# Kernel optimization log

Measured on AMD Instinct MI355X. Metric: run time of the kernel, lower is better.

The kernel has to match this reference:

```python
import jax, jax.numpy as jnp
import numpy as np

BS, TS, NE, ED = 32, 64, 64, 96
E = 256        # attn_embed_dim
H = 4          # attn_n_heads
HD = E // H    # head dim
RNN_H = 256
N_ACT = 32
NA = 16        # n_agents


def setup_inputs():
    key = jax.random.key(0)
    ks = jax.random.split(key, 40)
    entities = jax.random.normal(ks[0], (BS, TS, NE, ED), jnp.float32)
    obs_mask = jax.random.randint(ks[1], (BS, TS, NE, NE), 0, 2).astype(jnp.float32)  # 1 = masked
    entity_mask = (jax.random.uniform(ks[2], (BS, TS, NE)) < 0.1).astype(jnp.float32)  # 1 = inactive
    hidden_state = jnp.zeros((BS * NA, RNN_H), jnp.float32)
    it = iter(range(3, 40))
    def lin(fi, fo):
        return jax.random.normal(ks[next(it)], (fi, fo), jnp.float32) / np.sqrt(fi).astype(np.float32)
    p = dict(
        fc1_w=lin(ED, E), fc1_b=jnp.zeros((E,), jnp.float32),
        attn_in_w=lin(E, 3 * E), attn_out_w=lin(E, E), attn_out_b=jnp.zeros((E,), jnp.float32),
        fc2_w=lin(2 * E, RNN_H), fc2_b=jnp.zeros((RNN_H,), jnp.float32),
        gru_w_ih=lin(RNN_H, 3 * RNN_H), gru_w_hh=lin(RNN_H, 3 * RNN_H),
        gru_b_ih=jnp.zeros((3 * RNN_H,), jnp.float32), gru_b_hh=jnp.zeros((3 * RNN_H,), jnp.float32),
        fc3_w=lin(RNN_H, N_ACT), fc3_b=jnp.zeros((N_ACT,), jnp.float32),
        fcmsg1_w=lin(ED, E), fcmsg1_b=jnp.zeros((E,), jnp.float32),
        lmsg_in_w=lin(E, 3 * E), lmsg_out_w=lin(E, E), lmsg_out_b=jnp.zeros((E,), jnp.float32),
        gmsg_in_w=lin(E, 3 * E), gmsg_out_w=lin(E, E), gmsg_out_b=jnp.zeros((E,), jnp.float32),
        gate_in_w=lin(E, 3 * E), gate_out_w=lin(E, E), gate_out_b=jnp.zeros((E,), jnp.float32),
        gatefc1_w=lin(ED, E), gatefc1_b=jnp.zeros((E,), jnp.float32),
        gatefc2_w=lin(E, 2), gatefc2_b=jnp.zeros((2,), jnp.float32),
    )
    return dict(entities=entities, obs_mask=obs_mask, entity_mask=entity_mask,
                hidden_state=hidden_state, **p)


def _attn(x, in_w, out_w, out_b, pre_mask, post_mask):
    """REFIL EntityAttentionLayer: n_queries = NA agent rows, masks use 1 = masked."""
    B, ne, e = x.shape
    q, k, v = jnp.split(x @ in_w, 3, axis=-1)                       # each [B, ne, E]
    q = q[:, :NA].reshape(B, NA, H, HD).transpose(0, 2, 1, 3)        # [B, H, NA, HD]
    k = k.reshape(B, ne, H, HD).transpose(0, 2, 1, 3)                # [B, H, ne, HD]
    v = v.reshape(B, ne, H, HD).transpose(0, 2, 1, 3)
    logits = jnp.einsum('bhqd,bhkd->bhqk', q, k) / jnp.asarray(np.sqrt(HD), x.dtype)
    m = pre_mask[:, None, :NA, :]                                    # [B, 1, NA, ne]
    logits = jnp.where(m > 0, jnp.asarray(-1e9, x.dtype), logits)
    # softmax; zeroing masked cols also reproduces torch's NaN->0 for fully-masked rows
    w = jax.nn.softmax(logits, axis=-1) * (1.0 - m)
    out = jnp.einsum('bhqk,bhkd->bhqd', w, v).transpose(0, 2, 1, 3).reshape(B, NA, e)
    out = out @ out_w + out_b
    return out * (1.0 - post_mask[..., None])                        # masked_fill(post_mask, 0)


def _forward(entities, obs_mask, entity_mask, hidden_state,
             fc1_w, fc1_b, attn_in_w, attn_out_w, attn_out_b, fc2_w, fc2_b,
             gru_w_ih, gru_w_hh, gru_b_ih, gru_b_hh, fc3_w, fc3_b,
             fcmsg1_w, fcmsg1_b, lmsg_in_w, lmsg_out_w, lmsg_out_b,
             gmsg_in_w, gmsg_out_w, gmsg_out_b, gate_in_w, gate_out_w, gate_out_b,
             gatefc1_w, gatefc1_b, gatefc2_w, gatefc2_b):
    bs, ts, ne, ed = entities.shape
    B = bs * ts
    ent = entities.reshape(B, ne, ed)
    om = obs_mask.reshape(B, ne, ne)
    em = entity_mask.reshape(B, ne)
    agent_mask = em[:, :NA]                                          # [B, NA]
    full_obs_mask = 1.0 - (1.0 - agent_mask[:, None, :]) * (1.0 - agent_mask[:, :, None])

    x1 = jax.nn.relu(ent @ fc1_w + fc1_b)
    x2 = _attn(x1, attn_in_w, attn_out_w, attn_out_b, om, agent_mask)          # [B, NA, E]

    x1_msg = jax.nn.relu(ent @ fcmsg1_w + fcmsg1_b)
    x1_gate = jax.nn.relu(ent @ gatefc1_w + gatefc1_b)
    x2_msg = _attn(x1_msg, lmsg_in_w, lmsg_out_w, lmsg_out_b, om, agent_mask)  # [B, NA, E]
    x2_gate = _attn(x1_gate, gate_in_w, gate_out_w, gate_out_b, om, agent_mask)
    x2_gate = x2_gate @ gatefc2_w + gatefc2_b                                   # [B, NA, 2]

    # argmax of softmax == argmax of logits; gate in {0,1}, non-differentiable
    gate = jnp.argmax(x2_gate, axis=-1).astype(entities.dtype)
    gated_msg = x2_msg * gate[..., None]
    global_msg = _attn(gated_msg, gmsg_in_w, gmsg_out_w, gmsg_out_b,
                       full_obs_mask, agent_mask)                               # [B, NA, E]

    x3 = jax.nn.relu(jnp.concatenate([x2, global_msg], axis=-1) @ fc2_w + fc2_b)
    x3 = x3.reshape(bs, ts, NA, RNN_H)

    # GRU recurrence over ts via scan; hidden flattened to [bs*NA, RNN_H]
    h0 = hidden_state.reshape(-1, RNN_H)
    xs = x3.transpose(1, 0, 2, 3).reshape(ts, bs * NA, RNN_H)

    def step(h, x):
        gi = x @ gru_w_ih + gru_b_ih
        gh = h @ gru_w_hh + gru_b_hh
        ir, iz, inn = jnp.split(gi, 3, axis=-1)
        hr, hz, hn = jnp.split(gh, 3, axis=-1)
        r = jax.nn.sigmoid(ir + hr)
        z = jax.nn.sigmoid(iz + hz)
        n = jnp.tanh(inn + r * hn)
        h_new = (1.0 - z) * n + z * h
        return h_new, h_new

    _, hs = jax.lax.scan(step, h0, xs)                               # [ts, bs*NA, RNN_H]
    hs = hs.reshape(ts, bs, NA, RNN_H).transpose(1, 0, 2, 3)         # [bs, ts, NA, RNN_H]

    q = hs @ fc3_w + fc3_b                                           # [bs, ts, NA, N_ACT]
    am = agent_mask.reshape(bs, ts, NA, 1)
    q = q * (1.0 - am)                                               # masked_fill(agent_mask, 0)
    return q, hs, x2_gate


def reference(entities, obs_mask, entity_mask, hidden_state,
              fc1_w, fc1_b, attn_in_w, attn_out_w, attn_out_b, fc2_w, fc2_b,
              gru_w_ih, gru_w_hh, gru_b_ih, gru_b_hh, fc3_w, fc3_b,
              fcmsg1_w, fcmsg1_b, lmsg_in_w, lmsg_out_w, lmsg_out_b,
              gmsg_in_w, gmsg_out_w, gmsg_out_b, gate_in_w, gate_out_w, gate_out_b,
              gatefc1_w, gatefc1_b, gatefc2_w, gatefc2_b):
    return _forward(entities, obs_mask, entity_mask, hidden_state,
                    fc1_w, fc1_b, attn_in_w, attn_out_w, attn_out_b, fc2_w, fc2_b,
                    gru_w_ih, gru_w_hh, gru_b_ih, gru_b_hh, fc3_w, fc3_b,
                    fcmsg1_w, fcmsg1_b, lmsg_in_w, lmsg_out_w, lmsg_out_b,
                    gmsg_in_w, gmsg_out_w, gmsg_out_b, gate_in_w, gate_out_w, gate_out_b,
                    gatefc1_w, gatefc1_b, gatefc2_w, gatefc2_b)
```

## Files before the change

kernel.cpp:

```cpp
#include <hip/hip_runtime.h>


#define DEV __device__ __forceinline__

typedef _Float16 f16x8 __attribute__((ext_vector_type(8)));
typedef _Float16 f16x4 __attribute__((ext_vector_type(4)));
typedef float    f32x4 __attribute__((ext_vector_type(4)));
typedef float    f32x16 __attribute__((ext_vector_type(16)));

DEV f32x4 mfma16(f16x8 a, f16x8 b, f32x4 c){
  return __builtin_amdgcn_mfma_f32_16x16x32_f16(a, b, c, 0, 0, 0);
}
DEV f32x16 mfma32(f16x8 a, f16x8 b, f32x16 c){
  return __builtin_amdgcn_mfma_f32_32x32x16_f16(a, b, c, 0, 0, 0);
}

template<int MODE> struct AB {
  f16x8 hi, lo;
  DEV void mf(const AB& b, f32x4& c) const {
    if constexpr (MODE){
      c = mfma16(lo, b.hi, c);
      c = mfma16(hi, b.lo, c);
    }
    c = mfma16(hi, b.hi, c);
  }
};

template<int MODE> DEV AB<MODE> ldW(const _Float16* p, int losz){
  AB<MODE> r; r.hi = *(const f16x8*)p;
  if constexpr (MODE) r.lo = *(const f16x8*)(p + losz);
  return r;
}
template<int MODE> DEV AB<MODE> ldL(const _Float16* ph, const _Float16* pl){
  AB<MODE> r; r.hi = *(const f16x8*)ph;
  if constexpr (MODE) r.lo = *(const f16x8*)pl;
  return r;
}
template<int MODE> DEV AB<MODE> ldF(const float* p){
  AB<MODE> r;
  f32x4 v0 = *(const f32x4*)p, v1 = *(const f32x4*)(p + 4);
#pragma unroll
  for (int i = 0; i < 4; ++i){
    float a = v0[i], b = v1[i];
    _Float16 ah = (_Float16)a, bh = (_Float16)b;
    r.hi[i] = ah; r.hi[i+4] = bh;
    if constexpr (MODE){
      r.lo[i]   = (_Float16)(a - (float)ah);
      r.lo[i+4] = (_Float16)(b - (float)bh);
    }
  }
  return r;
}
template<int MODE> DEV void stL(_Float16* ph, _Float16* pl, int idx, float v){
  _Float16 h = (_Float16)v;
  ph[idx] = h;
  if constexpr (MODE) pl[idx] = (_Float16)(v - (float)h);
}

struct WJobs {
  const float* src[15];
  unsigned off[15];
  int K[15], N[15], mode[15];
};

__global__ __launch_bounds__(256) void k0_conv(WJobs jb, char* ws){
  const int job = blockIdx.y;
  const int K = jb.K[job], N = jb.N[job];
  const int total = K * N;
  _Float16* dh = (_Float16*)(ws + jb.off[job]);
  const float* src = jb.src[job];
  const int m = jb.mode[job];
  for (int idx = blockIdx.x*256 + threadIdx.x; idx < total; idx += gridDim.x*256){
    int n = idx / K, k = idx - n*K;
    float v = src[(size_t)k*N + n];
    _Float16 h = (_Float16)v;
    dh[idx] = h;
    if (m) dh[total + idx] = (_Float16)(v - (float)h);
  }
}

__global__ __launch_bounds__(256) void k0w_gate(
    const float* __restrict__ Wout, const float* __restrict__ Wg2,
    const float* __restrict__ bo,   const float* __restrict__ Win,
    _Float16* __restrict__ wveff, float* __restrict__ beff)
{
  __shared__ float weff_s[256*2];
  const int tid = threadIdx.x;
  {
    float a0 = 0.f, a1 = 0.f;
    const float* wr = Wout + (size_t)tid*256;
    for (int f = 0; f < 256; ++f){ float x = wr[f]; a0 += x*Wg2[2*f]; a1 += x*Wg2[2*f+1]; }
    weff_s[tid*2] = a0; weff_s[tid*2+1] = a1;
  }
  if (tid < 2){
    float s = 0.f;
    for (int f = 0; f < 256; ++f) s += bo[f]*Wg2[2*f + tid];
    beff[tid] = s;
  }
  __syncthreads();
  {
    const int j = tid;
    for (int n = 0; n < 16; ++n){
      float v = 0.f;
      if (n < 8){
        int h = n >> 1, c = n & 1;
        const float* wr = Win + (size_t)j*768 + 512 + h*64;
        const float* we = weff_s + (h*64)*2 + c;
        for (int d = 0; d < 64; ++d) v += wr[d]*we[2*d];
      }
      _Float16 hi = (_Float16)v;
      wveff[n*256 + j] = hi;
      wveff[16*256 + n*256 + j] = (_Float16)(v - (float)hi);
    }
  }
}

__global__ __launch_bounds__(512) void k1_all(
    const float* __restrict__ ent, const float* __restrict__ om, const float* __restrict__ em,
    const _Float16* __restrict__ W1a, const float* __restrict__ b1a,
    const _Float16* __restrict__ WINa,
    const _Float16* __restrict__ WOUTa, const float* __restrict__ boa,
    float* __restrict__ x2outa,
    const _Float16* __restrict__ W1b, const float* __restrict__ b1b,
    const _Float16* __restrict__ WINb,
    const _Float16* __restrict__ WOUTb, const float* __restrict__ bob,
    float* __restrict__ x2outb,
    const _Float16* __restrict__ W1g, const float* __restrict__ b1g,
    const _Float16* __restrict__ WINg,
    const _Float16* __restrict__ WVEFF,
    const float* __restrict__ beff, const float* __restrict__ gb2,
    float* __restrict__ og, float* __restrict__ gate)
{
  const int tid = threadIdx.x;
  const int w = tid >> 6, lg = (tid >> 4) & 3, li = tid & 15;
  extern __shared__ char smem[];

  if (blockIdx.x < 2048){
    const int br = blockIdx.x >> 10;
    const int p  = blockIdx.x & 1023;
    const int bb2[2] = { 2*p, 2*p + 1 };
    const _Float16* W1   = br ? W1b   : W1a;
    const float*    b1   = br ? b1b   : b1a;
    const _Float16* WIN  = br ? WINb  : WINa;
    const _Float16* WOUT = br ? WOUTb : WOUTa;
    const float*    bo   = br ? bob   : boa;
    float*          x2out= br ? x2outb: x2outa;

    const int wi = w & 3, ih = w >> 2;
    const int l = tid & 63;
    const int r32 = l & 31, kh = (l >> 5)*8;

    _Float16* x1   = (_Float16*)smem;
    _Float16* Ks   = (_Float16*)(smem + 67584);
    _Float16* Vs   = (_Float16*)(smem + 86016);
    _Float16* Qful = (_Float16*)(smem + 104448);
    float*    lgs  = (float*)(smem + 121344);
    _Float16* Ps   = (_Float16*)(smem + 130560);
    _Float16* outp = (_Float16*)(smem + 135168);

    {
      const int b = bb2[ih];
      _Float16* x1p = x1 + ih*16896;
      const int mt = wi & 1, ntb = (wi >> 1)*4;
      f32x16 acc0 = 0.f, acc1 = 0.f, acc2 = 0.f, acc3 = 0.f;
#pragma unroll
      for (int kk = 0; kk < 6; ++kk){
        AB<0> a = ldF<0>(ent + ((size_t)b*64 + mt*32 + r32)*96 + kk*16 + kh);
        f16x8 B0 = *(const f16x8*)(W1 + (size_t)((ntb + 0)*32 + r32)*96 + kk*16 + kh);
        f16x8 B1 = *(const f16x8*)(W1 + (size_t)((ntb + 1)*32 + r32)*96 + kk*16 + kh);
        f16x8 B2 = *(const f16x8*)(W1 + (size_t)((ntb + 2)*32 + r32)*96 + kk*16 + kh);
        f16x8 B3 = *(const f16x8*)(W1 + (size_t)((ntb + 3)*32 + r32)*96 + kk*16 + kh);
        acc0 = mfma32(a.hi, B0, acc0);
        acc1 = mfma32(a.hi, B1, acc1);
        acc2 = mfma32(a.hi, B2, acc2);
        acc3 = mfma32(a.hi, B3, acc3);
      }
#pragma unroll
      for (int s = 0; s < 4; ++s){
        const f32x16& ac = (s == 0) ? acc0 : (s == 1) ? acc1 : (s == 2) ? acc2 : acc3;
        int col = (ntb + s)*32 + r32;
        float bias = b1[col];
#pragma unroll
        for (int reg = 0; reg < 16; ++reg){
          int row = (reg & 3) + 8*(reg >> 2) + 4*(l >> 5);
          x1p[(mt*32 + row)*264 + col] = (_Float16)fmaxf(ac[reg] + bias, 0.f);
        }
      }
    }
    __syncthreads();

    {
      f32x16 acc = 0.f;
      const int itq = r32 >> 4, qr = r32 & 15;
      for (int kk = 0; kk < 16; ++kk){
        f16x8 A = *(const f16x8*)(x1 + itq*16896 + qr*264 + kk*16 + kh);
        f16x8 B = *(const f16x8*)(WIN + (size_t)(w*32 + r32)*256 + kk*16 + kh);
        acc = mfma32(A, B, acc);
      }
#pragma unroll
      for (int reg = 0; reg < 16; ++reg){
        int row = (reg & 3) + 8*(reg >> 2) + 4*(l >> 5);
        Qful[(row >> 4)*4224 + (row & 15)*264 + w*32 + r32] = (_Float16)acc[reg];
      }
    }
    __syncthreads();

    for (int h = 0; h < 4; ++h){
      if (w < 4){
        const int kt = w >> 1, dt = w & 1;
        f32x16 acc0 = 0.f, acc1 = 0.f;
        for (int kk = 0; kk < 16; ++kk){
          int ao = (kt*32 + r32)*264 + kk*16 + kh;
          f16x8 A0 = *(const f16x8*)(x1 + ao);
          f16x8 A1 = *(const f16x8*)(x1 + 16896 + ao);
          f16x8 B = *(const f16x8*)(WIN + (size_t)(256 + 64*h + dt*32 + r32)*256 + kk*16 + kh);
          acc0 = mfma32(A0, B, acc0);
          acc1 = mfma32(A1, B, acc1);
        }
#pragma unroll
        for (int reg = 0; reg < 16; ++reg){
          int row = (reg & 3) + 8*(reg >> 2) + 4*(l >> 5);
          Ks[(kt*32 + row)*72 + dt*32 + r32]        = (_Float16)acc0[reg];
          Ks[4608 + (kt*32 + row)*72 + dt*32 + r32] = (_Float16)acc1[reg];
        }
      } else {
        const int wv = w - 4;
        const int kt = wv >> 1, dt = wv & 1;
        f32x16 acc0 = 0.f, acc1 = 0.f;
        for (int kk = 0; kk < 16; ++kk){
          int ao = (kt*32 + r32)*264 + kk*16 + kh;
          f16x8 A0 = *(const f16x8*)(x1 + ao);
          f16x8 A1 = *(const f16x8*)(x1 + 16896 + ao);
          f16x8 B = *(const f16x8*)(WIN + (size_t)(512 + 64*h + dt*32 + r32)*256 + kk*16 + kh);
          acc0 = mfma32(A0, B, acc0);
          acc1 = mfma32(A1, B, acc1);
        }
#pragma unroll
        for (int rr = 0; rr < 4; ++rr){
          f16x4 p0, p1;
#pragma unroll
          for (int q4 = 0; q4 < 4; ++q4){
            p0[q4] = (_Float16)acc0[rr*4 + q4];
            p1[q4] = (_Float16)acc1[rr*4 + q4];
          }
          int key = kt*32 + rr*8 + 4*(l >> 5);
          *(f16x4*)(Vs + (dt*32 + r32)*72 + key)        = p0;
          *(f16x4*)(Vs + 4608 + (dt*32 + r32)*72 + key) = p1;
        }
      }
      __syncthreads();
      {
        const int b = bb2[ih];
        f32x4 acc = 0.f;
#pragma unroll
        for (int kk = 0; kk < 2; ++kk){
          f16x8 A = *(const f16x8*)(Qful + ih*4224 + li*264 + 64*h + kk*32 + lg*8);
          f16x8 B = *(const f16x8*)(Ks + ih*4608 + (16*wi + li)*72 + kk*32 + lg*8);
          acc = mfma16(A, B, acc);
        }
#pragma unroll
        for (int j = 0; j < 4; ++j){
          int q = 4*lg + j, key = 16*wi + li;
          float v = acc[j] * 0.125f;
          float m = om[((size_t)b*64 + q)*64 + key];
          if (m > 0.f) v = -1e9f;
          lgs[ih*1152 + q*72 + key] = v;
        }
      }
      __syncthreads();
      {
        const int it = tid >> 8, q = (tid >> 4) & 15, i16 = tid & 15;
        const int b = bb2[it];
        float pv[4], mx = -3e38f;
#pragma unroll
        for (int u = 0; u < 4; ++u){ pv[u] = lgs[it*1152 + q*72 + i16 + 16*u]; mx = fmaxf(mx, pv[u]); }
#pragma unroll
        for (int d = 1; d < 16; d <<= 1) mx = fmaxf(mx, __shfl_xor(mx, d, 16));
        float s = 0.f;
#pragma unroll
        for (int u = 0; u < 4; ++u){ pv[u] = expf(pv[u] - mx); s += pv[u]; }
#pragma unroll
        for (int d = 1; d < 16; d <<= 1) s += __shfl_xor(s, d, 16);
#pragma unroll
        for (int u = 0; u < 4; ++u){
          int key = i16 + 16*u;
          float m = om[((size_t)b*64 + q)*64 + key];
          Ps[it*1152 + q*72 + key] = (_Float16)((pv[u]/s)*(1.f - m));
        }
      }
      __syncthreads();
      {
        f32x4 acc = 0.f;
#pragma unroll
        for (int kk = 0; kk < 2; ++kk){
          f16x8 A = *(const f16x8*)(Ps + ih*1152 + li*72 + kk*32 + lg*8);
          f16x8 B = *(const f16x8*)(Vs + ih*4608 + (16*wi + li)*72 + kk*32 + lg*8);
          acc = mfma16(A, B, acc);
        }
#pragma unroll
        for (int j = 0; j < 4; ++j)
          outp[ih*4224 + (4*lg + j)*264 + 64*h + 16*wi + li] = (_Float16)acc[j];
      }
      __syncthreads();
    }

    {
      f32x16 acc = 0.f;
      const int ito = r32 >> 4, qr = r32 & 15;
      for (int kk = 0; kk < 16; ++kk){
        f16x8 A = *(const f16x8*)(outp + ito*4224 + qr*264 + kk*16 + kh);
        f16x8 B = *(const f16x8*)(WOUT + (size_t)(w*32 + r32)*256 + kk*16 + kh);
        acc = mfma32(A, B, acc);
      }
      int col = w*32 + r32;
      float bias = bo[col];
#pragma unroll
      for (int reg = 0; reg < 16; ++reg){
        int row = (reg & 3) + 8*(reg >> 2) + 4*(l >> 5);
        int it2 = row >> 4, q2 = row & 15;
        const int b = bb2[it2];
        float v = (acc[reg] + bias) * (1.f - em[(size_t)b*64 + q2]);
        x2out[((size_t)b*16 + q2)*256 + col] = v;
      }
    }
    return;
  }

  {
    constexpr int W1SZ = 96*256, WINSZ = 256*768, WVSZ = 16*256;
    const int b = blockIdx.x - 2048;
    const int l = tid & 63;
    const int r32 = l & 31, kh = (l >> 5)*8;

    char* sp = smem;
    _Float16* x1h = (_Float16*)sp; sp += 64*264*2;
    _Float16* x1l = (_Float16*)sp; sp += 64*264*2;
    _Float16* Kh  = (_Float16*)sp; sp += 64*72*2;
    _Float16* Kl  = (_Float16*)sp; sp += 64*72*2;
    _Float16* Qh  = (_Float16*)sp; sp += 16*264*2;
    _Float16* Ql  = (_Float16*)sp; sp += 16*264*2;
    float*    lgs = (float*)sp;    sp += 16*72*4;
    float*    Ps  = (float*)sp;    sp += 16*66*4;
    float*    v2s = (float*)sp;    sp += 64*18*4;
    float*  ogacc = (float*)sp;    sp += 32*4;
    float*  Kpart = (float*)sp;    sp += 8192*4;

    {
      const int mt = w & 1, ntb = (w >> 1)*2;
      f32x16 acc0 = 0.f, acc1 = 0.f;
#pragma unroll
      for (int kk = 0; kk < 6; ++kk){
        AB<1> a = ldF<1>(ent + ((size_t)b*64 + mt*32 + r32)*96 + kk*16 + kh);
#pragma unroll
        for (int s = 0; s < 2; ++s){
          const _Float16* bp = W1g + (size_t)((ntb + s)*32 + r32)*96 + kk*16 + kh;
          f16x8 Bh = *(const f16x8*)bp;
          f16x8 Bl = *(const f16x8*)(bp + W1SZ);
          f32x16& ac = s ? acc1 : acc0;
          ac = mfma32(a.lo, Bh, ac);
          ac = mfma32(a.hi, Bl, ac);
          ac = mfma32(a.hi, Bh, ac);
        }
      }
#pragma unroll
      for (int s = 0; s < 2; ++s){
        const f32x16& ac = s ? acc1 : acc0;
        int col = (ntb + s)*32 + r32;
        float bias = b1g[col];
#pragma unroll
        for (int reg = 0; reg < 16; ++reg){
          int row = (reg & 3) + 8*(reg >> 2) + 4*(l >> 5);
          stL<1>(x1h, x1l, (mt*32 + row)*264 + col, fmaxf(ac[reg] + bias, 0.f));
        }
      }
    }
    if (tid < 32) ogacc[tid] = 0.f;
    __syncthreads();

    {
#pragma unroll
      for (int s = 0; s < 2; ++s){
        int nt = w + s*8;
        f32x4 acc = 0.f;
        for (int kk = 0; kk < 8; ++kk){
          int ao = li*264 + kk*32 + lg*8;
          AB<1> a = ldL<1>(x1h + ao, x1l + ao);
          AB<1> bb = ldW<1>(WINg + (size_t)(nt*16 + li)*256 + kk*32 + lg*8, WINSZ);
          a.mf(bb, acc);
        }
#pragma unroll
        for (int j = 0; j < 4; ++j)
          stL<1>(Qh, Ql, (4*lg + j)*264 + nt*16 + li, acc[j]);
      }
      if (w < 4){
        f32x4 acc = 0.f;
        for (int kk = 0; kk < 8; ++kk){
          int ao = (w*16 + li)*264 + kk*32 + lg*8;
          AB<1> a = ldL<1>(x1h + ao, x1l + ao);
          AB<1> bb = ldW<1>(WVEFF + (size_t)li*256 + kk*32 + lg*8, WVSZ);
          a.mf(bb, acc);
        }
#pragma unroll
        for (int j = 0; j < 4; ++j)
          v2s[(w*16 + 4*lg + j)*18 + li] = acc[j];
      }
    }
    __syncthreads();

    for (int h = 0; h < 4; ++h){
      {
        const int t = w & 3, kt = t >> 1, dt = t & 1, khalf = w >> 2;
        f32x16 acc = 0.f;
#pragma unroll
        for (int k8 = 0; k8 < 8; ++k8){
          int ko = (khalf*8 + k8)*16 + kh;
          int ao = (kt*32 + r32)*264 + ko;
          f16x8 ah = *(const f16x8*)(x1h + ao);
          f16x8 al = *(const f16x8*)(x1l + ao);
          const _Float16* bp = WINg + (size_t)(256 + h*64 + dt*32 + r32)*256 + ko;
          f16x8 Bh = *(const f16x8*)bp;
          f16x8 Bl = *(const f16x8*)(bp + WINSZ);
          acc = mfma32(al, Bh, acc);
          acc = mfma32(ah, Bl, acc);
          acc = mfma32(ah, Bh, acc);
        }
#pragma unroll
        for (int reg = 0; reg < 16; ++reg){
          int row = (reg & 3) + 8*(reg >> 2) + 4*(l >> 5);
          Kpart[((khalf*4 + t)*32 + row)*32 + r32] = acc[reg];
        }
      }
      __syncthreads();
      {
        for (int e = tid; e < 4096; e += 512){
          float s2 = Kpart[e] + Kpart[4096 + e];
          int t2 = e >> 10, idx = e & 1023, row = idx >> 5, col = idx & 31;
          stL<1>(Kh, Kl, ((t2 >> 1)*32 + row)*72 + (t2 & 1)*32 + col, s2);
        }
      }
      __syncthreads();
      if (w < 4){
        f32x4 acc = 0.f;
#pragma unroll
        for (int kk = 0; kk < 2; ++kk){
          int ao = li*264 + h*64 + kk*32 + lg*8;
          AB<1> a = ldL<1>(Qh + ao, Ql + ao);
          int bo_ = (16*w + li)*72 + kk*32 + lg*8;
          AB<1> bb = ldL<1>(Kh + bo_, Kl + bo_);
          a.mf(bb, acc);
        }
#pragma unroll
        for (int j = 0; j < 4; ++j){
          int q = 4*lg + j, key = 16*w + li;
          float v = acc[j] * 0.125f;
          float m = om[((size_t)b*64 + q)*64 + key];
          if (m > 0.f) v = -1e9f;
          lgs[q*72 + key] = v;
        }
      }
      __syncthreads();
      if (tid < 256){
        int q = tid >> 4, i16 = tid & 15;
        float pv[4], mx = -3e38f;
#pragma unroll
        for (int u = 0; u < 4; ++u){ pv[u] = lgs[q*72 + i16 + 16*u]; mx = fmaxf(mx, pv[u]); }
#pragma unroll
        for (int d = 1; d < 16; d <<= 1) mx = fmaxf(mx, __shfl_xor(mx, d, 16));
        float s = 0.f;
#pragma unroll
        for (int u = 0; u < 4; ++u){ pv[u] = expf(pv[u] - mx); s += pv[u]; }
#pragma unroll
        for (int d = 1; d < 16; d <<= 1) s += __shfl_xor(s, d, 16);
#pragma unroll
        for (int u = 0; u < 4; ++u){
          int key = i16 + 16*u;
          float m = om[((size_t)b*64 + q)*64 + key];
          Ps[q*66 + key] = (pv[u]/s)*(1.f - m);
        }
      }
      __syncthreads();
      if (tid < 256){
        int q = tid >> 4, l16 = tid & 15;
        float a0 = 0.f, a1 = 0.f;
#pragma unroll
        for (int u = 0; u < 4; ++u){
          int k = l16 + 16*u;
          float p2 = Ps[q*66 + k];
          a0 += p2 * v2s[k*18 + h*2];
          a1 += p2 * v2s[k*18 + h*2 + 1];
        }
#pragma unroll
        for (int d = 1; d < 16; d <<= 1){ a0 += __shfl_xor(a0, d, 16); a1 += __shfl_xor(a1, d, 16); }
        if (l16 == 0){ ogacc[q*2] += a0; ogacc[q*2 + 1] += a1; }
      }
      __syncthreads();
    }
    if (tid < 16){
      int q = tid;
      float am = em[(size_t)b*64 + q];
      float g0 = (1.f - am)*(ogacc[2*q]     + beff[0]) + gb2[0];
      float g1 = (1.f - am)*(ogacc[2*q + 1] + beff[1]) + gb2[1];
      og[((size_t)b*16 + q)*2]     = g0;
      og[((size_t)b*16 + q)*2 + 1] = g1;
      gate[(size_t)b*16 + q] = (g1 > g0) ? 1.f : 0.f;
    }
  }
}

__global__ __launch_bounds__(512) void k2_global(
    const float* __restrict__ em,
    const float* __restrict__ x2, const float* __restrict__ x2m,
    const float* __restrict__ gate,
    const _Float16* __restrict__ GMIN, const _Float16* __restrict__ GMOUT, const float* __restrict__ gob,
    const _Float16* __restrict__ FC2T, const float* __restrict__ fc2b,
    const _Float16* __restrict__ GIHT, const float* __restrict__ gib,
    float* __restrict__ gi)
{
  const int p = blockIdx.x;
  const int tid = threadIdx.x;
  const int w = tid >> 6, lg = (tid >> 4) & 3, li = tid & 15;
  const int l = tid & 63;
  const int r32 = l & 31, kh = (l >> 5)*8;

  extern __shared__ char smem[];
  float*    gate_s = (float*)smem;
  _Float16* gm_s   = (_Float16*)(smem + 128);
  float*    lg2    = (float*)(smem + 17024);
  _Float16* P2     = (_Float16*)(smem + 20096);
  _Float16* outp   = (_Float16*)(smem + 22656);
  _Float16* x3_s   = (_Float16*)(smem + 39552);
  _Float16* Vtall  = (_Float16*)(smem + 56448);
  _Float16* Qall   = (_Float16*)(smem + 97408);
  _Float16* Kall   = (_Float16*)(smem + 114304);
  _Float16* cat_s  = (_Float16*)(smem + 97408);

  if (tid < 32){
    int it = tid >> 4, q = tid & 15;
    gate_s[it*16 + q] = gate[(size_t)(2*p + it)*16 + q];
  }
  __syncthreads();
#pragma unroll
  for (int it = 0; it < 2; ++it){
    const int b = 2*p + it;
    for (int idx = tid; idx < 4096; idx += 512){
      int q = idx >> 8, d = idx & 255;
      gm_s[it*4224 + q*264 + d] = (_Float16)(x2m[((size_t)b*16 + q)*256 + d] * gate_s[it*16 + q]);
    }
  }
  for (int idx = tid; idx < 10240; idx += 512) ((unsigned*)Vtall)[idx] = 0u;
  for (int idx = tid; idx < 2*16*40; idx += 512) P2[idx] = (_Float16)0.f;
  __syncthreads();

  {
    const int itq = r32 >> 4, qr = r32 & 15;
#pragma unroll
    for (int s = 0; s < 3; ++s){
      int nt = 3*w + s;
      f32x16 acc = 0.f;
      for (int kk = 0; kk < 16; ++kk){
        f16x8 A = *(const f16x8*)(gm_s + itq*4224 + qr*264 + kk*16 + kh);
        f16x8 B = *(const f16x8*)(GMIN + (size_t)(nt*32 + r32)*256 + kk*16 + kh);
        acc = mfma32(A, B, acc);
      }
      int sec = nt >> 3;
      int hcol = (nt & 7)*32 + r32;
#pragma unroll
      for (int reg = 0; reg < 16; ++reg){
        int row = (reg & 3) + 8*(reg >> 2) + 4*(l >> 5);
        int it2 = row >> 4, q2 = row & 15;
        _Float16 v = (_Float16)acc[reg];
        if (sec == 0)      Qall[it2*4224 + q2*264 + hcol] = v;
        else if (sec == 1) Kall[it2*4224 + q2*264 + hcol] = v;
        else               Vtall[it2*10240 + hcol*40 + q2] = v;
      }
    }
  }
  __syncthreads();

  for (int h = 0; h < 4; ++h){
    if (w < 2){
      const int it = w, b = 2*p + it;
      f32x4 acc = 0.f;
#pragma unroll
      for (int kk = 0; kk < 2; ++kk){
        f16x8 A = *(const f16x8*)(Qall + it*4224 + li*264 + 64*h + kk*32 + lg*8);
        f16x8 B = *(const f16x8*)(Kall + it*4224 + li*264 + 64*h + kk*32 + lg*8);
        acc = mfma16(A, B, acc);
      }
      float amk = em[(size_t)b*64 + li];
#pragma unroll
      for (int j = 0; j < 4; ++j){
        int q = 4*lg + j;
        float amq = em[(size_t)b*64 + q];
        float m = 1.f - (1.f - amq)*(1.f - amk);
        float v = acc[j]*0.125f;
        if (m > 0.f) v = -1e9f;
        lg2[it*384 + q*24 + li] = v;
      }
    }
    __syncthreads();
    if (tid < 256){
      int q = tid >> 4, key = tid & 15;
#pragma unroll
      for (int it = 0; it < 2; ++it){
        const int b = 2*p + it;
        float v = lg2[it*384 + q*24 + key];
        float mx = v;
#pragma unroll
        for (int d = 1; d < 16; d <<= 1) mx = fmaxf(mx, __shfl_xor(mx, d, 16));
        float pe = expf(v - mx);
        float s = pe;
#pragma unroll
        for (int d = 1; d < 16; d <<= 1) s += __shfl_xor(s, d, 16);
        float amq = em[(size_t)b*64 + q], amk = em[(size_t)b*64 + key];
        float m = 1.f - (1.f - amq)*(1.f - amk);
        P2[it*640 + q*40 + key] = (_Float16)((pe/s)*(1.f - m));
      }
    }
    __syncthreads();
    {
      const int it = w & 1, dt = w >> 1;
      f32x4 acc = 0.f;
      f16x8 A = *(const f16x8*)(P2 + it*640 + li*40 + lg*8);
      f16x8 B = *(const f16x8*)(Vtall + it*10240 + (size_t)(64*h + 16*dt + li)*40 + lg*8);
      acc = mfma16(A, B, acc);
#pragma unroll
      for (int j = 0; j < 4; ++j)
        outp[it*4224 + (4*lg + j)*264 + 64*h + 16*dt + li] = (_Float16)acc[j];
    }
    __syncthreads();
  }
  {
    const int ito = r32 >> 4, qr = r32 & 15;
    {
      int nt = w;
      f32x16 acc = 0.f;
      for (int kk = 0; kk < 16; ++kk){
        f16x8 A = *(const f16x8*)(outp + ito*4224 + qr*264 + kk*16 + kh);
        f16x8 B = *(const f16x8*)(GMOUT + (size_t)(nt*32 + r32)*256 + kk*16 + kh);
        acc = mfma32(A, B, acc);
      }
      int col = nt*32 + r32;
      float bias = gob[col];
#pragma unroll
      for (int reg = 0; reg < 16; ++reg){
        int row = (reg & 3) + 8*(reg >> 2) + 4*(l >> 5);
        int it2 = row >> 4, q2 = row & 15;
        float m = 1.f - em[(size_t)(2*p + it2)*64 + q2];
        cat_s[it2*8320 + q2*520 + 256 + col] = (_Float16)((acc[reg] + bias)*m);
      }
    }
#pragma unroll
    for (int it = 0; it < 2; ++it){
      const int b = 2*p + it;
      for (int idx = tid; idx < 4096; idx += 512){
        int q = idx >> 8, d = idx & 255;
        cat_s[it*8320 + q*520 + d] = (_Float16)(x2[((size_t)b*16 + q)*256 + d]);
      }
    }
  }
  __syncthreads();
  {
    const int ito = r32 >> 4, qr = r32 & 15;
    int nt = w;
    f32x16 acc = 0.f;
    for (int kk = 0; kk < 32; ++kk){
      f16x8 A = *(const f16x8*)(cat_s + ito*8320 + qr*520 + kk*16 + kh);
      f16x8 B = *(const f16x8*)(FC2T + (size_t)(nt*32 + r32)*512 + kk*16 + kh);
      acc = mfma32(A, B, acc);
    }
    int col = nt*32 + r32;
    float bias = fc2b[col];
#pragma unroll
    for (int reg = 0; reg < 16; ++reg){
      int row = (reg & 3) + 8*(reg >> 2) + 4*(l >> 5);
      int it2 = row >> 4, q2 = row & 15;
      x3_s[it2*4224 + q2*264 + col] = (_Float16)fmaxf(acc[reg] + bias, 0.f);
    }
  }
  __syncthreads();
  {
    const int r0 = ((2*p) >> 6)*16, t0 = (2*p) & 63;
    const int ito = r32 >> 4, qr = r32 & 15;
#pragma unroll
    for (int s = 0; s < 3; ++s){
      int nt = 3*w + s;
      f32x16 acc = 0.f;
      for (int kk = 0; kk < 16; ++kk){
        f16x8 A = *(const f16x8*)(x3_s + ito*4224 + qr*264 + kk*16 + kh);
        f16x8 B = *(const f16x8*)(GIHT + (size_t)(nt*32 + r32)*256 + kk*16 + kh);
        acc = mfma32(A, B, acc);
      }
      int col = nt*32 + r32;
      float bias = gib[col];
#pragma unroll
      for (int reg = 0; reg < 16; ++reg){
        int row = (reg & 3) + 8*(reg >> 2) + 4*(l >> 5);
        int it2 = row >> 4, q2 = row & 15;
        gi[((size_t)((r0 + q2)*64 + t0 + it2))*768 + col] = acc[reg] + bias;
      }
    }
  }
}

__global__ __launch_bounds__(512) void k3_gru(
    const _Float16* __restrict__ WHH, const float* __restrict__ bhh,
    const float* __restrict__ gi, const float* __restrict__ h0,
    float* __restrict__ hs)
{
  const int rb = blockIdx.x;
  const int row0 = rb * 16;
  const int tid = threadIdx.x;
  const int w = tid >> 6, lg = (tid >> 4) & 3, li = tid & 15;

  extern __shared__ char smem3[];
  _Float16* hf16 = (_Float16*)smem3;
  float* hf32 = (float*)(smem3 + 8448);
  float* gh   = (float*)(smem3 + 8448 + 16640);
  float* bhs  = (float*)(smem3 + 8448 + 16640 + 49664);

  for (int idx = tid; idx < 768; idx += 512) bhs[idx] = bhh[idx];
  for (int idx = tid; idx < 4096; idx += 512){
    int r = idx >> 8, d = idx & 255;
    float v = h0[(size_t)(row0 + r)*256 + d];
    hf32[r*260 + d] = v;
    hf16[r*264 + d] = (_Float16)v;
  }
  __syncthreads();

  const int er = tid >> 5;
  const int dd = (tid & 31) * 8;

  for (int t = 0; t < 64; ++t){
    const float* gp = gi + ((size_t)(row0 + er)*64 + t)*768 + dd;
    f32x4 gr[2], gz[2], gn[2];
#pragma unroll
    for (int v = 0; v < 2; ++v){
      gr[v] = *(const f32x4*)(gp + v*4);
      gz[v] = *(const f32x4*)(gp + 256 + v*4);
      gn[v] = *(const f32x4*)(gp + 512 + v*4);
    }
    f16x8 a[8];
#pragma unroll
    for (int kk = 0; kk < 8; ++kk)
      a[kk] = *(const f16x8*)(hf16 + li*264 + kk*32 + lg*8);
    f32x4 acc[6];
#pragma unroll
    for (int c = 0; c < 6; ++c) acc[c] = 0.f;
#pragma unroll
    for (int c = 0; c < 6; ++c){
      const _Float16* bp = WHH + (size_t)(w*96 + c*16 + li)*256 + lg*8;
#pragma unroll
      for (int kk = 0; kk < 8; ++kk)
        acc[c] = mfma16(a[kk], *(const f16x8*)(bp + kk*32), acc[c]);
    }
#pragma unroll
    for (int c = 0; c < 6; ++c){
      int col = w*96 + c*16 + li;
#pragma unroll
      for (int j = 0; j < 4; ++j)
        gh[(4*lg + j)*776 + col] = acc[c][j];
    }
    __syncthreads();
    {
      float* hp32 = hf32 + er*260 + dd;
      float* hsp  = hs + ((size_t)(rb*64 + t)*16 + er)*256 + dd;
      f16x8 hv8;
#pragma unroll
      for (int v = 0; v < 2; ++v){
        f32x4 xr = *(const f32x4*)(gh + er*776 +       dd + v*4);
        f32x4 xz = *(const f32x4*)(gh + er*776 + 256 + dd + v*4);
        f32x4 xn = *(const f32x4*)(gh + er*776 + 512 + dd + v*4);
        f32x4 hold = *(const f32x4*)(hp32 + v*4);
        f32x4 hout;
#pragma unroll
        for (int e = 0; e < 4; ++e){
          int d = dd + v*4 + e;
          float rr_ = 1.f/(1.f + __expf(-(gr[v][e] + xr[e] + bhs[d])));
          float zz  = 1.f/(1.f + __expf(-(gz[v][e] + xz[e] + bhs[256 + d])));
          float pre = gn[v][e] + rr_*(xn[e] + bhs[512 + d]);
          float nn  = 1.f - 2.f/(1.f + __expf(2.f*pre));
          float hv = (1.f - zz)*nn + zz*hold[e];
          hout[e] = hv;
          hv8[v*4 + e] = (_Float16)hv;
        }
        *(f32x4*)(hp32 + v*4) = hout;
        *(f32x4*)(hsp + v*4)  = hout;
      }
      *(f16x8*)(hf16 + er*264 + dd) = hv8;
    }
    __syncthreads();
  }
}

__global__ __launch_bounds__(256) void k4_q(
    const _Float16* __restrict__ FC3T, const float* __restrict__ fc3b,
    const float* __restrict__ em, const float* __restrict__ hs, float* __restrict__ qo)
{
  const int tid = threadIdx.x;
  const int w = tid >> 6, lg = (tid >> 4) & 3, li = tid & 15;
  const int rb = blockIdx.x*64 + 16*w;
  f32x4 acc[2];
#pragma unroll
  for (int c = 0; c < 2; ++c) acc[c] = 0.f;
  for (int kk = 0; kk < 8; ++kk){
    const float* ap = hs + (size_t)(rb + li)*256 + kk*32 + lg*8;
    f32x4 v0 = *(const f32x4*)ap, v1 = *(const f32x4*)(ap + 4);
    f16x8 A;
#pragma unroll
    for (int e = 0; e < 4; ++e){ A[e] = (_Float16)v0[e]; A[e+4] = (_Float16)v1[e]; }
#pragma unroll
    for (int c = 0; c < 2; ++c){
      f16x8 B = *(const f16x8*)(FC3T + (size_t)(16*c + li)*256 + kk*32 + lg*8);
      acc[c] = mfma16(A, B, acc[c]);
    }
  }
#pragma unroll
  for (int c = 0; c < 2; ++c){
    int col = 16*c + li;
    float bias = fc3b[col];
#pragma unroll
    for (int j = 0; j < 4; ++j){
      int row = rb + 4*lg + j;
      float am = em[(size_t)(row >> 4)*64 + (row & 15)];
      qo[(size_t)row*32 + col] = (acc[c][j] + bias)*(1.f - am);
    }
  }
}

extern "C" void kernel_launch(void* const* d_in, const int* in_sizes, int n_in,
                              void* d_out, int out_size, void* d_ws, size_t ws_size,
                              hipStream_t stream)
{
  constexpr size_t OFF_FC1T   = 0;
  constexpr size_t OFF_MSG1T  = 49152;
  constexpr size_t OFF_AINT   = 98304;
  constexpr size_t OFF_LINT   = 491520;
  constexpr size_t OFF_AOUTT  = 884736;
  constexpr size_t OFF_LOUTT  = 1015808;
  constexpr size_t OFF_GMINT  = 1146880;
  constexpr size_t OFF_GMOUTT = 1540096;
  constexpr size_t OFF_FC2T   = 1671168;
  constexpr size_t OFF_GIHT   = 1933312;
  constexpr size_t OFF_GHHT   = 2326528;
  constexpr size_t OFF_FC3T   = 2719744;
  constexpr size_t OFF_G1T    = 2736128;
  constexpr size_t OFF_GINT   = 2834432;
  constexpr size_t OFF_WVEFF  = 3620864;
  constexpr size_t OFF_BEFF   = 3637248;
  constexpr size_t OFF_GATE   = 3637504;
  constexpr size_t OFF_X2     = 3768576;
  constexpr size_t OFF_X2M    = 37323008;
  constexpr size_t OFF_GI     = 70877440;
  constexpr size_t NEED       = 171540736;
  if (ws_size < NEED) return;

  char* ws = (char*)d_ws;
  const float* ent = (const float*)d_in[0];
  const float* om  = (const float*)d_in[1];
  const float* em  = (const float*)d_in[2];

  WJobs jb{};
  int nj = 0;
  auto addj = [&](int src_idx, size_t off, int K, int N, int m){
    jb.src[nj] = (const float*)d_in[src_idx]; jb.off[nj] = (unsigned)off;
    jb.K[nj] = K; jb.N[nj] = N; jb.mode[nj] = m; ++nj;
  };
  addj(4,  OFF_FC1T,   96, 256, 0);
  addj(17, OFF_MSG1T,  96, 256, 0);
  addj(6,  OFF_AINT,  256, 768, 0);
  addj(19, OFF_LINT,  256, 768, 0);
  addj(7,  OFF_AOUTT, 256, 256, 0);
  addj(20, OFF_LOUTT, 256, 256, 0);
  addj(22, OFF_GMINT, 256, 768, 0);
  addj(23, OFF_GMOUTT,256, 256, 0);
  addj(9,  OFF_FC2T,  512, 256, 0);
  addj(11, OFF_GIHT,  256, 768, 0);
  addj(12, OFF_GHHT,  256, 768, 0);
  addj(15, OFF_FC3T,  256,  32, 0);
  addj(28, OFF_G1T,    96, 256, 1);
  addj(25, OFF_GINT,  256, 768, 1);
  k0_conv<<<dim3(96, nj), 256, 0, stream>>>(jb, ws);

  k0w_gate<<<1, 256, 0, stream>>>(
      (const float*)d_in[26], (const float*)d_in[30],
      (const float*)d_in[27], (const float*)d_in[25],
      (_Float16*)(ws + OFF_WVEFF), (float*)(ws + OFF_BEFF));

  constexpr int SMB = 156672, SMK2 = 131200, SM3 = 77824;
  (void)hipFuncSetAttribute(reinterpret_cast<const void*>(&k1_all),
                            hipFuncAttributeMaxDynamicSharedMemorySize, SMB);
  (void)hipFuncSetAttribute(reinterpret_cast<const void*>(&k2_global),
                            hipFuncAttributeMaxDynamicSharedMemorySize, SMK2);
  (void)hipFuncSetAttribute(reinterpret_cast<const void*>(&k3_gru),
                            hipFuncAttributeMaxDynamicSharedMemorySize, SM3);

  float* qout = (float*)d_out;
  float* hsout = qout + 1048576;
  float* gout = qout + 9437184;

  k1_all<<<4096, 512, SMB, stream>>>(ent, om, em,
      (const _Float16*)(ws + OFF_FC1T),  (const float*)d_in[5],
      (const _Float16*)(ws + OFF_AINT),
      (const _Float16*)(ws + OFF_AOUTT), (const float*)d_in[8],
      (float*)(ws + OFF_X2),
      (const _Float16*)(ws + OFF_MSG1T), (const float*)d_in[18],
      (const _Float16*)(ws + OFF_LINT),
      (const _Float16*)(ws + OFF_LOUTT), (const float*)d_in[21],
      (float*)(ws + OFF_X2M),
      (const _Float16*)(ws + OFF_G1T),   (const float*)d_in[29],
      (const _Float16*)(ws + OFF_GINT),
      (const _Float16*)(ws + OFF_WVEFF),
      (const float*)(ws + OFF_BEFF), (const float*)d_in[31],
      gout, (float*)(ws + OFF_GATE));

  k2_global<<<1024, 512, SMK2, stream>>>(em,
      (const float*)(ws + OFF_X2), (const float*)(ws + OFF_X2M),
      (const float*)(ws + OFF_GATE),
      (const _Float16*)(ws + OFF_GMINT), (const _Float16*)(ws + OFF_GMOUTT), (const float*)d_in[24],
      (const _Float16*)(ws + OFF_FC2T), (const float*)d_in[10],
      (const _Float16*)(ws + OFF_GIHT), (const float*)d_in[13],
      (float*)(ws + OFF_GI));

  k3_gru<<<32, 512, SM3, stream>>>(
      (const _Float16*)(ws + OFF_GHHT), (const float*)d_in[14],
      (const float*)(ws + OFF_GI), (const float*)d_in[3], hsout);

  k4_q<<<512, 256, 0, stream>>>(
      (const _Float16*)(ws + OFF_FC3T), (const float*)d_in[16],
      em, hsout, qout);
}
```

Before: 1.074 ms.

## Fuse GRU gate math into MFMA accumulators and double-buffer hidden state

```diff
diff --git a/kernel.cpp b/kernel.cpp
--- a/kernel.cpp
+++ b/kernel.cpp
@@ -714,80 +714,77 @@
   const int w = tid >> 6, lg = (tid >> 4) & 3, li = tid & 15;
 
   extern __shared__ char smem3[];
-  _Float16* hf16 = (_Float16*)smem3;
-  float* hf32 = (float*)(smem3 + 8448);
-  float* gh   = (float*)(smem3 + 8448 + 16640);
-  float* bhs  = (float*)(smem3 + 8448 + 16640 + 49664);
+  _Float16* hbuf = (_Float16*)smem3;
+  float*    bhs  = (float*)(smem3 + 16896);
 
   for (int idx = tid; idx < 768; idx += 512) bhs[idx] = bhh[idx];
   for (int idx = tid; idx < 4096; idx += 512){
     int r = idx >> 8, d = idx & 255;
-    float v = h0[(size_t)(row0 + r)*256 + d];
-    hf32[r*260 + d] = v;
-    hf16[r*264 + d] = (_Float16)v;
-  }
+    hbuf[r*264 + d] = (_Float16)h0[(size_t)(row0 + r)*256 + d];
+  }
+  float hreg[4][2];
+#pragma unroll
+  for (int j = 0; j < 4; ++j)
+#pragma unroll
+    for (int c = 0; c < 2; ++c)
+      hreg[j][c] = h0[(size_t)(row0 + 4*lg + j)*256 + w*32 + c*16 + li];
   __syncthreads();
 
-  const int er = tid >> 5;
-  const int dd = (tid & 31) * 8;
+  float bR[2], bZ[2], bN[2];
+#pragma unroll
+  for (int c = 0; c < 2; ++c){
+    int d = w*32 + c*16 + li;
+    bR[c] = bhs[d]; bZ[c] = bhs[256 + d]; bN[c] = bhs[512 + d];
+  }
 
   for (int t = 0; t < 64; ++t){
-    const float* gp = gi + ((size_t)(row0 + er)*64 + t)*768 + dd;
-    f32x4 gr[2], gz[2], gn[2];
-#pragma unroll
-    for (int v = 0; v < 2; ++v){
-      gr[v] = *(const f32x4*)(gp + v*4);
-      gz[v] = *(const f32x4*)(gp + 256 + v*4);
-      gn[v] = *(const f32x4*)(gp + 512 + v*4);
+    const _Float16* hb = hbuf + (t & 1)*4224;
+    _Float16*       hn = hbuf + ((t + 1) & 1)*4224;
+    float gr[4][2], gz[4][2], gn_[4][2];
+#pragma unroll
+    for (int j = 0; j < 4; ++j){
+      const float* gp = gi + ((size_t)(row0 + 4*lg + j)*64 + t)*768 + w*32 + li;
+#pragma unroll
+      for (int c = 0; c < 2; ++c){
+        gr[j][c]  = gp[c*16];
+        gz[j][c]  = gp[256 + c*16];
+        gn_[j][c] = gp[512 + c*16];
+      }
     }
     f16x8 a[8];
 #pragma unroll
     for (int kk = 0; kk < 8; ++kk)
-      a[kk] = *(const f16x8*)(hf16 + li*264 + kk*32 + lg*8);
-    f32x4 acc[6];
-#pragma unroll
-    for (int c = 0; c < 6; ++c) acc[c] = 0.f;
-#pragma unroll
-    for (int c = 0; c < 6; ++c){
-      const _Float16* bp = WHH + (size_t)(w*96 + c*16 + li)*256 + lg*8;
-#pragma unroll
-      for (int kk = 0; kk < 8; ++kk)
-        acc[c] = mfma16(a[kk], *(const f16x8*)(bp + kk*32), acc[c]);
-    }
-#pragma unroll
-    for (int c = 0; c < 6; ++c){
-      int col = w*96 + c*16 + li;
-#pragma unroll
-      for (int j = 0; j < 4; ++j)
-        gh[(4*lg + j)*776 + col] = acc[c][j];
-    }
-    __syncthreads();
-    {
-      float* hp32 = hf32 + er*260 + dd;
-      float* hsp  = hs + ((size_t)(rb*64 + t)*16 + er)*256 + dd;
-      f16x8 hv8;
-#pragma unroll
-      for (int v = 0; v < 2; ++v){
-        f32x4 xr = *(const f32x4*)(gh + er*776 +       dd + v*4);
-        f32x4 xz = *(const f32x4*)(gh + er*776 + 256 + dd + v*4);
-        f32x4 xn = *(const f32x4*)(gh + er*776 + 512 + dd + v*4);
-        f32x4 hold = *(const f32x4*)(hp32 + v*4);
-        f32x4 hout;
-#pragma unroll
-        for (int e = 0; e < 4; ++e){
-          int d = dd + v*4 + e;
-          float rr_ = 1.f/(1.f + __expf(-(gr[v][e] + xr[e] + bhs[d])));
-          float zz  = 1.f/(1.f + __expf(-(gz[v][e] + xz[e] + bhs[256 + d])));
-          float pre = gn[v][e] + rr_*(xn[e] + bhs[512 + d]);
-          float nn  = 1.f - 2.f/(1.f + __expf(2.f*pre));
-          float hv = (1.f - zz)*nn + zz*hold[e];
-          hout[e] = hv;
-          hv8[v*4 + e] = (_Float16)hv;
-        }
-        *(f32x4*)(hp32 + v*4) = hout;
-        *(f32x4*)(hsp + v*4)  = hout;
-      }
-      *(f16x8*)(hf16 + er*264 + dd) = hv8;
+      a[kk] = *(const f16x8*)(hb + li*264 + kk*32 + lg*8);
+    f32x4 aR[2], aZ[2], aN[2];
+#pragma unroll
+    for (int c = 0; c < 2; ++c){ aR[c] = 0.f; aZ[c] = 0.f; aN[c] = 0.f; }
+#pragma unroll
+    for (int c = 0; c < 2; ++c){
+      const _Float16* bpR = WHH + (size_t)(      w*32 + c*16 + li)*256 + lg*8;
+      const _Float16* bpZ = WHH + (size_t)(256 + w*32 + c*16 + li)*256 + lg*8;
+      const _Float16* bpN = WHH + (size_t)(512 + w*32 + c*16 + li)*256 + lg*8;
+#pragma unroll
+      for (int kk = 0; kk < 8; ++kk){
+        aR[c] = mfma16(a[kk], *(const f16x8*)(bpR + kk*32), aR[c]);
+        aZ[c] = mfma16(a[kk], *(const f16x8*)(bpZ + kk*32), aZ[c]);
+        aN[c] = mfma16(a[kk], *(const f16x8*)(bpN + kk*32), aN[c]);
+      }
+    }
+    float* hsp_base = hs + ((size_t)(rb*64 + t)*16)*256;
+#pragma unroll
+    for (int j = 0; j < 4; ++j){
+#pragma unroll
+      for (int c = 0; c < 2; ++c){
+        int d = w*32 + c*16 + li;
+        float rr_ = 1.f/(1.f + __expf(-(gr[j][c] + aR[c][j] + bR[c])));
+        float zz  = 1.f/(1.f + __expf(-(gz[j][c] + aZ[c][j] + bZ[c])));
+        float pre = gn_[j][c] + rr_*(aN[c][j] + bN[c]);
+        float nn  = 1.f - 2.f/(1.f + __expf(2.f*pre));
+        float hv = (1.f - zz)*nn + zz*hreg[j][c];
+        hreg[j][c] = hv;
+        hsp_base[(size_t)(4*lg + j)*256 + d] = hv;
+        hn[(4*lg + j)*264 + d] = (_Float16)hv;
+      }
     }
     __syncthreads();
   }
@@ -887,7 +884,7 @@
       (const float*)d_in[27], (const float*)d_in[25],
       (_Float16*)(ws + OFF_WVEFF), (float*)(ws + OFF_BEFF));
 
-  constexpr int SMB = 156672, SMK2 = 131200, SM3 = 77824;
+  constexpr int SMB = 156672, SMK2 = 131200, SM3 = 19968;
   (void)hipFuncSetAttribute(reinterpret_cast<const void*>(&k1_all),
                             hipFuncAttributeMaxDynamicSharedMemorySize, SMB);
   (void)hipFuncSetAttribute(reinterpret_cast<const void*>(&k2_global),
```

Result: slower. 1.251 ms (+16.5%).
